# Kernel optimization log

Hardware: AMD Instinct MI355X
Metric: run time of the kernel (lower is better)

## Reference

```python
import jax, jax.numpy as jnp
import numpy as np

N_NODES = 100000
N_EDGES = 1600000
D_IN = 64
D_HID = 64
N_LAYERS = 3


def setup_inputs() -> dict:
    key = jax.random.key(0)
    ks = jax.random.split(key, 10)
    inp = {
        "node_feat": jax.random.normal(ks[0], (N_NODES, D_IN), dtype=jnp.float32),
        "src": jax.random.randint(ks[1], (N_EDGES,), 0, N_NODES, dtype=jnp.int32),
        "dst": jax.random.randint(ks[2], (N_EDGES,), 0, N_NODES, dtype=jnp.int32),
        "graph_len": jnp.ones((1,), dtype=jnp.int32) * N_NODES,
    }
    # GraphConv weights: shape (in_feats, out_feats), applied as feat @ W + b (DGL xavier-style init)
    dims = [D_IN] + [D_HID] * N_LAYERS
    for i in range(N_LAYERS):
        scale = float(np.sqrt(2.0 / (dims[i] + dims[i + 1])))
        inp[f"W{i}"] = jax.random.normal(ks[3 + i], (dims[i], dims[i + 1]), dtype=jnp.float32) * scale
        inp[f"b{i}"] = jnp.zeros((dims[i + 1],), dtype=jnp.float32)
    return inp


def reference(node_feat, src, dst, graph_len, W0, b0, W1, b1, W2, b2):
    n = node_feat.shape[0]
    e = src.shape[0]
    ones = jnp.ones((e,), dtype=node_feat.dtype)
    # DGL GraphConv norm='both': src-side out-degree^{-1/2}, dst-side in-degree^{-1/2}, clamp(min=1)
    deg_out = jax.ops.segment_sum(ones, src, num_segments=n)
    deg_in = jax.ops.segment_sum(ones, dst, num_segments=n)
    inv_sqrt_out = jax.lax.rsqrt(jnp.clip(deg_out, 1.0, None))[:, None]  # [N,1]
    inv_sqrt_in = jax.lax.rsqrt(jnp.clip(deg_in, 1.0, None))[:, None]    # [N,1]

    def graph_conv(x, W, b):
        msg = (x * inv_sqrt_out)[src]                              # [E,F] gather
        agg = jax.ops.segment_sum(msg, dst, num_segments=n)        # [N,F] scatter-add
        return (agg * inv_sqrt_in) @ W + b                         # SpMM result -> dense linear

    xs = []
    h = node_feat
    for W, b in ((W0, b0), (W1, b1), (W2, b2)):
        h = jax.nn.relu(graph_conv(h, W, b))
        xs.append(h)

    # Faithful to source: torch.sum(x, dim=1) -> per-node scalar [N]; concat over layers -> [3N]
    x_pool = jnp.concatenate([x.sum(axis=1) for x in xs], axis=-1)
    xs_cat = jnp.concatenate(xs, axis=-1)  # [N, 3*H]
    return x_pool, xs_cat
```

## Files before the change

kernel.cpp:

```cpp
#include <hip/hip_runtime.h>


#define TPB 256
#define CAPB 16384
#define CAP_S2 10240

__device__ __forceinline__ unsigned short f2bf(float f) {
  unsigned u = __float_as_uint(f);
  u += 0x7fff + ((u >> 16) & 1);
  return (unsigned short)(u >> 16);
}
__device__ __forceinline__ float bflo(unsigned u) { return __uint_as_float(u << 16); }
__device__ __forceinline__ float bfhi(unsigned u) { return __uint_as_float(u & 0xffff0000u); }

__global__ void init_cursors(int* __restrict__ cur_s, int* __restrict__ cur_d) {
  int t = threadIdx.x;
  cur_s[t] = t * CAPB;
  cur_d[t] = t * CAPB;
}

__global__ __launch_bounds__(256) void scatter_both(
    const int* __restrict__ src, const int* __restrict__ dst, int e,
    int* __restrict__ cur_s, int* __restrict__ cur_d,
    int* __restrict__ srcbuf, unsigned* __restrict__ edges1) {
  __shared__ int hs[256], hd[256];
  int t = threadIdx.x, b = blockIdx.x;
  hs[t] = 0; hd[t] = 0;
  __syncthreads();
  int base = b * 4096;
  int sv[16], dv[16];
  #pragma unroll
  for (int k = 0; k < 4; k++) {
    int i = base + 4 * t + 1024 * k;
    if (i + 3 < e) {
      int4 s4 = *(const int4*)&src[i];
      int4 d4 = *(const int4*)&dst[i];
      sv[4*k] = s4.x; sv[4*k+1] = s4.y; sv[4*k+2] = s4.z; sv[4*k+3] = s4.w;
      dv[4*k] = d4.x; dv[4*k+1] = d4.y; dv[4*k+2] = d4.z; dv[4*k+3] = d4.w;
    } else {
      #pragma unroll
      for (int j = 0; j < 4; j++) {
        int idx = i + j;
        if (idx < e) { sv[4*k+j] = src[idx]; dv[4*k+j] = dst[idx]; }
        else { sv[4*k+j] = -1; dv[4*k+j] = -1; }
      }
    }
  }
  #pragma unroll
  for (int k = 0; k < 16; k++) {
    if (dv[k] >= 0) {
      atomicAdd(&hs[sv[k] >> 9], 1);
      atomicAdd(&hd[dv[k] >> 9], 1);
    }
  }
  __syncthreads();
  int bs = hs[t], bd = hd[t];
  hs[t] = bs ? atomicAdd(&cur_s[t], bs) : 0;
  hd[t] = bd ? atomicAdd(&cur_d[t], bd) : 0;
  __syncthreads();
  #pragma unroll
  for (int k = 0; k < 16; k++) {
    if (dv[k] >= 0) {
      int ps = atomicAdd(&hs[sv[k] >> 9], 1);
      srcbuf[ps] = sv[k];
      int pd = atomicAdd(&hd[dv[k] >> 9], 1);
      edges1[pd] = ((unsigned)sv[k] << 9) | (unsigned)(dv[k] & 511);
    }
  }
}

__global__ __launch_bounds__(256) void sort_deg_cast(
    const unsigned* __restrict__ edges1, const int* __restrict__ srcbuf,
    const int* __restrict__ cur_s, const int* __restrict__ cur_d,
    const float* __restrict__ node_feat,
    int2* __restrict__ row_be,
    float* __restrict__ inv_in, float* __restrict__ inv_out,
    unsigned short* __restrict__ xb, int* __restrict__ col, int n) {
  __shared__ int sOut[CAP_S2];
  __shared__ int hist[512], cur[512];
  __shared__ int psum[256];
  __shared__ int dhist[512];
  __shared__ float sInv[512];
  int b = blockIdx.x, t = threadIdx.x;
  int sbase = b * CAPB;
  int es = cur_s[b];
  int ed = cur_d[b];
  int rstart = b << 9;
  int nrows = min(512, n - rstart);
  hist[t] = 0; hist[t + 256] = 0;
  dhist[t] = 0; dhist[t + 256] = 0;
  __syncthreads();
  for (int i = sbase + t; i < ed; i += TPB) atomicAdd(&hist[edges1[i] & 511u], 1);
  for (int i = sbase + t; i < es; i += TPB) atomicAdd(&dhist[srcbuf[i] & 511], 1);
  __syncthreads();
  #pragma unroll
  for (int k = 0; k < 2; k++) {
    int r = t + k * 256;
    if (r < nrows) {
      float iv = rsqrtf(fmaxf((float)dhist[r], 1.0f));
      sInv[r] = iv;
      inv_out[rstart + r] = iv;
    }
  }
  int h0 = hist[2 * t], h1 = hist[2 * t + 1];
  psum[t] = h0 + h1; __syncthreads();
  for (int off = 1; off < 256; off <<= 1) {
    int a = (t >= off) ? psum[t - off] : 0;
    __syncthreads(); psum[t] += a; __syncthreads();
  }
  int ex = psum[t] - (h0 + h1);
  cur[2 * t] = ex; cur[2 * t + 1] = ex + h0;
  if (2 * t < nrows) {
    row_be[rstart + 2 * t] = make_int2(sbase + ex, sbase + ex + h0);
    inv_in[rstart + 2 * t] = rsqrtf(fmaxf((float)h0, 1.0f));
  }
  if (2 * t + 1 < nrows) {
    row_be[rstart + 2 * t + 1] = make_int2(sbase + ex + h0, sbase + ex + h0 + h1);
    inv_in[rstart + 2 * t + 1] = rsqrtf(fmaxf((float)h1, 1.0f));
  }
  __syncthreads();
  for (int i = sbase + t; i < ed; i += TPB) {
    unsigned v = edges1[i];
    int pos = atomicAdd(&cur[v & 511u], 1);
    int svv = (int)(v >> 9);
    if (pos < CAP_S2) sOut[pos] = svv;
    else col[sbase + pos] = svv;
  }
  __syncthreads();
  int m = min(ed - sbase, CAP_S2);
  for (int k = t; k < m; k += TPB) col[sbase + k] = sOut[k];
  int total4 = nrows * 16;
  const float* xbase = node_feat + (size_t)rstart * 64;
  unsigned short* obase = xb + (size_t)rstart * 64;
  for (int u = t; u < total4; u += TPB) {
    int r = u >> 4;
    float sc = sInv[r];
    float4 v = *(const float4*)&xbase[(size_t)u * 4];
    ushort4 o;
    o.x = f2bf(v.x * sc); o.y = f2bf(v.y * sc);
    o.z = f2bf(v.z * sc); o.w = f2bf(v.w * sc);
    *(ushort4*)&obase[(size_t)u * 4] = o;
  }
}

__global__ __launch_bounds__(512) void spmm_gemm(
    const unsigned short* __restrict__ xb,
    const int2* __restrict__ row_be,
    const int* __restrict__ col,
    const float* __restrict__ inv_in, const float* __restrict__ inv_out,
    const float* __restrict__ W, const float* __restrict__ bias,
    float* __restrict__ out_cat, float* __restrict__ out_pool,
    unsigned short* __restrict__ xb_next, int n) {
  __shared__ float sXT[64][68];
  int t = threadIdx.x;
  int row0 = blockIdx.x << 6;
  int lane = t & 63;
  int g = lane >> 3;
  int l8 = (lane & 7) << 3;
  int wv = t >> 6;
  for (int k = 0; k < 8; k++) {
    int rl = wv * 8 + k;
    int row = row0 + rl;
    float v = 0.f;
    if (row < n) {
      int2 be = row_be[row];
      int s = be.x, e = be.y;
      float inv = inv_in[row];
      float a0 = 0, a1 = 0, a2 = 0, a3 = 0, a4 = 0, a5 = 0, a6 = 0, a7 = 0;
      int ec = e - 1;
      for (int i = s + g; i < e; i += 16) {
        int i1 = i + 8;
        int c0 = col[i];
        int c1 = col[min(i1, ec)];
        float m1 = (i1 < e) ? 1.f : 0.f;
        uint4 r0 = *(const uint4*)&xb[(size_t)c0 * 64 + l8];
        uint4 r1 = *(const uint4*)&xb[(size_t)c1 * 64 + l8];
        a0 += bflo(r0.x); a1 += bfhi(r0.x); a2 += bflo(r0.y); a3 += bfhi(r0.y);
        a4 += bflo(r0.z); a5 += bfhi(r0.z); a6 += bflo(r0.w); a7 += bfhi(r0.w);
        a0 = fmaf(m1, bflo(r1.x), a0); a1 = fmaf(m1, bfhi(r1.x), a1);
        a2 = fmaf(m1, bflo(r1.y), a2); a3 = fmaf(m1, bfhi(r1.y), a3);
        a4 = fmaf(m1, bflo(r1.z), a4); a5 = fmaf(m1, bfhi(r1.z), a5);
        a6 = fmaf(m1, bflo(r1.w), a6); a7 = fmaf(m1, bfhi(r1.w), a7);
      }
      a0 += __shfl_xor(a0, 8); a0 += __shfl_xor(a0, 16); a0 += __shfl_xor(a0, 32);
      a1 += __shfl_xor(a1, 8); a1 += __shfl_xor(a1, 16); a1 += __shfl_xor(a1, 32);
      a2 += __shfl_xor(a2, 8); a2 += __shfl_xor(a2, 16); a2 += __shfl_xor(a2, 32);
      a3 += __shfl_xor(a3, 8); a3 += __shfl_xor(a3, 16); a3 += __shfl_xor(a3, 32);
      a4 += __shfl_xor(a4, 8); a4 += __shfl_xor(a4, 16); a4 += __shfl_xor(a4, 32);
      a5 += __shfl_xor(a5, 8); a5 += __shfl_xor(a5, 16); a5 += __shfl_xor(a5, 32);
      a6 += __shfl_xor(a6, 8); a6 += __shfl_xor(a6, 16); a6 += __shfl_xor(a6, 32);
      a7 += __shfl_xor(a7, 8); a7 += __shfl_xor(a7, 16); a7 += __shfl_xor(a7, 32);
      float s0 = (g & 1) ? a1 : a0;
      float s1 = (g & 1) ? a3 : a2;
      float s2 = (g & 1) ? a5 : a4;
      float s3 = (g & 1) ? a7 : a6;
      float u0 = (g & 2) ? s1 : s0;
      float u1 = (g & 2) ? s3 : s2;
      v = ((g & 4) ? u1 : u0) * inv;
    }
    sXT[l8 + g][rl] = v;
  }
  __syncthreads();
  int tj = t & 15, tr = t >> 4;
  int j4 = tj << 2, r2 = tr << 1;
  const float4 bv = *(const float4*)&bias[j4];
  float4 a0 = bv, a1 = bv;
  #pragma unroll 8
  for (int f = 0; f < 64; f++) {
    float4 w  = *(const float4*)&W[f * 64 + j4];
    float2 xv = *(const float2*)&sXT[f][r2];
    a0.x = fmaf(xv.x, w.x, a0.x); a0.y = fmaf(xv.x, w.y, a0.y);
    a0.z = fmaf(xv.x, w.z, a0.z); a0.w = fmaf(xv.x, w.w, a0.w);
    a1.x = fmaf(xv.y, w.x, a1.x); a1.y = fmaf(xv.y, w.y, a1.y);
    a1.z = fmaf(xv.y, w.z, a1.z); a1.w = fmaf(xv.y, w.w, a1.w);
  }
  float4 accs[2] = {a0, a1};
  #pragma unroll
  for (int ri = 0; ri < 2; ri++) {
    int row = row0 + r2 + ri;
    if (row < n) {
      float4 h = accs[ri];
      h.x = fmaxf(h.x, 0.f); h.y = fmaxf(h.y, 0.f);
      h.z = fmaxf(h.z, 0.f); h.w = fmaxf(h.w, 0.f);
      *(float4*)&out_cat[(size_t)row * 192 + j4] = h;
      if (xb_next) {
        float sc = inv_out[row];
        ushort4 o;
        o.x = f2bf(h.x * sc); o.y = f2bf(h.y * sc);
        o.z = f2bf(h.z * sc); o.w = f2bf(h.w * sc);
        *(ushort4*)&xb_next[(size_t)row * 64 + j4] = o;
      }
      float part = h.x + h.y + h.z + h.w;
      part += __shfl_xor(part, 1);
      part += __shfl_xor(part, 2);
      part += __shfl_xor(part, 4);
      part += __shfl_xor(part, 8);
      if (tj == 0) out_pool[row] = part;
    }
  }
}


extern "C" void kernel_launch(void* const* d_in, const int* in_sizes, int n_in,
                              void* d_out, int out_size, void* d_ws, size_t ws_size,
                              hipStream_t stream) {
  const float* node_feat = (const float*)d_in[0];
  const int* src = (const int*)d_in[1];
  const int* dst = (const int*)d_in[2];
  const float* Ws[3] = {(const float*)d_in[4], (const float*)d_in[6], (const float*)d_in[8]};
  const float* bs[3] = {(const float*)d_in[5], (const float*)d_in[7], (const float*)d_in[9]};
  float* out = (float*)d_out;
  int n = in_sizes[0] / 64;
  int e = in_sizes[1];
  int nbb = (n + 511) >> 9;
  int nblk = (e + 4095) / 4096;
  size_t slots = (size_t)nbb * CAPB;

  char* p = (char*)d_ws;
  unsigned short* xba = (unsigned short*)p; p += (size_t)n * 64 * sizeof(unsigned short);
  unsigned short* xbb = (unsigned short*)p; p += (size_t)n * 64 * sizeof(unsigned short);
  float* inv_out = (float*)p;   p += (size_t)n * sizeof(float);
  float* inv_in = (float*)p;    p += (size_t)n * sizeof(float);
  int2* row_be = (int2*)p;      p += (size_t)n * sizeof(int2);
  int* cur_s = (int*)p;         p += 256 * sizeof(int);
  int* cur_d = (int*)p;         p += 256 * sizeof(int);
  unsigned* edges1 = (unsigned*)p; p += slots * sizeof(unsigned);
  int* srcbuf = (int*)p;        p += slots * sizeof(int);
  int* col = (int*)p;           p += slots * sizeof(int);

  init_cursors<<<1, 256, 0, stream>>>(cur_s, cur_d);
  scatter_both<<<nblk, TPB, 0, stream>>>(src, dst, e, cur_s, cur_d, srcbuf, edges1);
  sort_deg_cast<<<nbb, TPB, 0, stream>>>(edges1, srcbuf, cur_s, cur_d, node_feat,
                                         row_be, inv_in, inv_out, xba, col, n);

  float* cat_base = out + (size_t)3 * n;
  int nfb = (n + 63) >> 6;
  spmm_gemm<<<nfb, 512, 0, stream>>>(xba, row_be, col, inv_in, inv_out,
      Ws[0], bs[0], cat_base + 0 * 64, out + (size_t)0 * n, xbb, n);
  spmm_gemm<<<nfb, 512, 0, stream>>>(xbb, row_be, col, inv_in, inv_out,
      Ws[1], bs[1], cat_base + 1 * 64, out + (size_t)1 * n, xba, n);
  spmm_gemm<<<nfb, 512, 0, stream>>>(xba, row_be, col, inv_in, inv_out,
      Ws[2], bs[2], cat_base + 2 * 64, out + (size_t)2 * n, (unsigned short*)nullptr, n);
}
```

Measured before the change: 367.4 us.

## Compute out-degree with global atomics and shrink dst buckets to 256 rows

The out-degree bucketing pass (srcbuf scatter plus a per-bucket histogram) is replaced by direct global atomicAdd into a per-node deg_out array. Destination buckets shrink from 512 to 256 rows, so the sort kernel runs with twice as many blocks and half the shared-memory staging. The bf16 cast and scaling move into a separate grid-stride kernel. This removes one edge-sized scatter and read, but adds 1.6M global atomics and an extra kernel launch.

```diff
diff --git a/kernel.cpp b/kernel.cpp
--- a/kernel.cpp
+++ b/kernel.cpp
@@ -2,8 +2,8 @@
 
 
 #define TPB 256
-#define CAPB 16384
-#define CAP_S2 10240
+#define CAPB 8192
+#define CAP_S2 5120
 
 __device__ __forceinline__ unsigned short f2bf(float f) {
   unsigned u = __float_as_uint(f);
@@ -13,19 +13,23 @@
 __device__ __forceinline__ float bflo(unsigned u) { return __uint_as_float(u << 16); }
 __device__ __forceinline__ float bfhi(unsigned u) { return __uint_as_float(u & 0xffff0000u); }
 
-__global__ void init_cursors(int* __restrict__ cur_s, int* __restrict__ cur_d) {
+__global__ void init_zero(int* __restrict__ deg_out, int* __restrict__ cur_d, int n) {
   int t = threadIdx.x;
-  cur_s[t] = t * CAPB;
-  cur_d[t] = t * CAPB;
+  if (blockIdx.x == 0) {
+    cur_d[t] = t * CAPB;
+    cur_d[t + 256] = (t + 256) * CAPB;
+  }
+  int idx = blockIdx.x * 256 + t;
+  if (idx < n) deg_out[idx] = 0;
 }
 
 __global__ __launch_bounds__(256) void scatter_both(
     const int* __restrict__ src, const int* __restrict__ dst, int e,
-    int* __restrict__ cur_s, int* __restrict__ cur_d,
-    int* __restrict__ srcbuf, unsigned* __restrict__ edges1) {
-  __shared__ int hs[256], hd[256];
+    int* __restrict__ cur_d, int* __restrict__ deg_out,
+    unsigned* __restrict__ edges1) {
+  __shared__ int hd[512];
   int t = threadIdx.x, b = blockIdx.x;
-  hs[t] = 0; hd[t] = 0;
+  hd[t] = 0; hd[t + 256] = 0;
   __syncthreads();
   int base = b * 4096;
   int sv[16], dv[16];
@@ -49,97 +53,81 @@
   #pragma unroll
   for (int k = 0; k < 16; k++) {
     if (dv[k] >= 0) {
-      atomicAdd(&hs[sv[k] >> 9], 1);
-      atomicAdd(&hd[dv[k] >> 9], 1);
-    }
-  }
-  __syncthreads();
-  int bs = hs[t], bd = hd[t];
-  hs[t] = bs ? atomicAdd(&cur_s[t], bs) : 0;
-  hd[t] = bd ? atomicAdd(&cur_d[t], bd) : 0;
+      atomicAdd(&hd[dv[k] >> 8], 1);
+      atomicAdd(&deg_out[sv[k]], 1);
+    }
+  }
+  __syncthreads();
+  #pragma unroll
+  for (int k = 0; k < 2; k++) {
+    int bin = t + 256 * k;
+    int bd = hd[bin];
+    hd[bin] = bd ? atomicAdd(&cur_d[bin], bd) : 0;
+  }
   __syncthreads();
   #pragma unroll
   for (int k = 0; k < 16; k++) {
     if (dv[k] >= 0) {
-      int ps = atomicAdd(&hs[sv[k] >> 9], 1);
-      srcbuf[ps] = sv[k];
-      int pd = atomicAdd(&hd[dv[k] >> 9], 1);
-      edges1[pd] = ((unsigned)sv[k] << 9) | (unsigned)(dv[k] & 511);
-    }
-  }
-}
-
-__global__ __launch_bounds__(256) void sort_deg_cast(
-    const unsigned* __restrict__ edges1, const int* __restrict__ srcbuf,
-    const int* __restrict__ cur_s, const int* __restrict__ cur_d,
-    const float* __restrict__ node_feat,
-    int2* __restrict__ row_be,
-    float* __restrict__ inv_in, float* __restrict__ inv_out,
-    unsigned short* __restrict__ xb, int* __restrict__ col, int n) {
+      int pd = atomicAdd(&hd[dv[k] >> 8], 1);
+      edges1[pd] = ((unsigned)sv[k] << 8) | (unsigned)(dv[k] & 255);
+    }
+  }
+}
+
+__global__ __launch_bounds__(256) void sort_place(
+    const unsigned* __restrict__ edges1, const int* __restrict__ cur_d,
+    int2* __restrict__ row_be, float* __restrict__ inv_in,
+    int* __restrict__ col, int n) {
   __shared__ int sOut[CAP_S2];
-  __shared__ int hist[512], cur[512];
-  __shared__ int psum[256];
-  __shared__ int dhist[512];
-  __shared__ float sInv[512];
+  __shared__ int hist[256], cur[256], psum[256];
   int b = blockIdx.x, t = threadIdx.x;
   int sbase = b * CAPB;
-  int es = cur_s[b];
   int ed = cur_d[b];
-  int rstart = b << 9;
-  int nrows = min(512, n - rstart);
-  hist[t] = 0; hist[t + 256] = 0;
-  dhist[t] = 0; dhist[t + 256] = 0;
-  __syncthreads();
-  for (int i = sbase + t; i < ed; i += TPB) atomicAdd(&hist[edges1[i] & 511u], 1);
-  for (int i = sbase + t; i < es; i += TPB) atomicAdd(&dhist[srcbuf[i] & 511], 1);
-  __syncthreads();
-  #pragma unroll
-  for (int k = 0; k < 2; k++) {
-    int r = t + k * 256;
-    if (r < nrows) {
-      float iv = rsqrtf(fmaxf((float)dhist[r], 1.0f));
-      sInv[r] = iv;
-      inv_out[rstart + r] = iv;
-    }
-  }
-  int h0 = hist[2 * t], h1 = hist[2 * t + 1];
-  psum[t] = h0 + h1; __syncthreads();
+  int rstart = b << 8;
+  int nrows = min(256, n - rstart);
+  hist[t] = 0;
+  __syncthreads();
+  for (int i = sbase + t; i < ed; i += TPB) atomicAdd(&hist[edges1[i] & 255u], 1);
+  __syncthreads();
+  int h0 = hist[t];
+  psum[t] = h0; __syncthreads();
   for (int off = 1; off < 256; off <<= 1) {
     int a = (t >= off) ? psum[t - off] : 0;
     __syncthreads(); psum[t] += a; __syncthreads();
   }
-  int ex = psum[t] - (h0 + h1);
-  cur[2 * t] = ex; cur[2 * t + 1] = ex + h0;
-  if (2 * t < nrows) {
-    row_be[rstart + 2 * t] = make_int2(sbase + ex, sbase + ex + h0);
-    inv_in[rstart + 2 * t] = rsqrtf(fmaxf((float)h0, 1.0f));
-  }
-  if (2 * t + 1 < nrows) {
-    row_be[rstart + 2 * t + 1] = make_int2(sbase + ex + h0, sbase + ex + h0 + h1);
-    inv_in[rstart + 2 * t + 1] = rsqrtf(fmaxf((float)h1, 1.0f));
-  }
+  int ex = psum[t] - h0;
+  if (t < nrows) {
+    row_be[rstart + t] = make_int2(sbase + ex, sbase + ex + h0);
+    inv_in[rstart + t] = rsqrtf(fmaxf((float)h0, 1.0f));
+  }
+  cur[t] = ex;
   __syncthreads();
   for (int i = sbase + t; i < ed; i += TPB) {
     unsigned v = edges1[i];
-    int pos = atomicAdd(&cur[v & 511u], 1);
-    int svv = (int)(v >> 9);
+    int pos = atomicAdd(&cur[v & 255u], 1);
+    int svv = (int)(v >> 8);
     if (pos < CAP_S2) sOut[pos] = svv;
     else col[sbase + pos] = svv;
   }
   __syncthreads();
   int m = min(ed - sbase, CAP_S2);
   for (int k = t; k < m; k += TPB) col[sbase + k] = sOut[k];
-  int total4 = nrows * 16;
-  const float* xbase = node_feat + (size_t)rstart * 64;
-  unsigned short* obase = xb + (size_t)rstart * 64;
-  for (int u = t; u < total4; u += TPB) {
+}
+
+__global__ __launch_bounds__(256) void cast_xb(
+    const float* __restrict__ node_feat, const int* __restrict__ deg_out,
+    float* __restrict__ inv_out, unsigned short* __restrict__ xb, int n) {
+  int total4 = n * 16;
+  int stride = gridDim.x * 256;
+  for (int u = blockIdx.x * 256 + threadIdx.x; u < total4; u += stride) {
     int r = u >> 4;
-    float sc = sInv[r];
-    float4 v = *(const float4*)&xbase[(size_t)u * 4];
+    float iv = rsqrtf(fmaxf((float)deg_out[r], 1.0f));
+    if ((u & 15) == 0) inv_out[r] = iv;
+    float4 v = *(const float4*)&node_feat[(size_t)u * 4];
     ushort4 o;
-    o.x = f2bf(v.x * sc); o.y = f2bf(v.y * sc);
-    o.z = f2bf(v.z * sc); o.w = f2bf(v.w * sc);
-    *(ushort4*)&obase[(size_t)u * 4] = o;
+    o.x = f2bf(v.x * iv); o.y = f2bf(v.y * iv);
+    o.z = f2bf(v.z * iv); o.w = f2bf(v.w * iv);
+    *(ushort4*)&xb[(size_t)u * 4] = o;
   }
 }
 
@@ -252,7 +240,7 @@
   float* out = (float*)d_out;
   int n = in_sizes[0] / 64;
   int e = in_sizes[1];
-  int nbb = (n + 511) >> 9;
+  int nbb = (n + 255) >> 8;
   int nblk = (e + 4095) / 4096;
   size_t slots = (size_t)nbb * CAPB;
 
@@ -262,16 +250,15 @@
   float* inv_out = (float*)p;   p += (size_t)n * sizeof(float);
   float* inv_in = (float*)p;    p += (size_t)n * sizeof(float);
   int2* row_be = (int2*)p;      p += (size_t)n * sizeof(int2);
-  int* cur_s = (int*)p;         p += 256 * sizeof(int);
-  int* cur_d = (int*)p;         p += 256 * sizeof(int);
+  int* deg_out = (int*)p;       p += (size_t)n * sizeof(int);
+  int* cur_d = (int*)p;         p += 512 * sizeof(int);
   unsigned* edges1 = (unsigned*)p; p += slots * sizeof(unsigned);
-  int* srcbuf = (int*)p;        p += slots * sizeof(int);
   int* col = (int*)p;           p += slots * sizeof(int);
 
-  init_cursors<<<1, 256, 0, stream>>>(cur_s, cur_d);
-  scatter_both<<<nblk, TPB, 0, stream>>>(src, dst, e, cur_s, cur_d, srcbuf, edges1);
-  sort_deg_cast<<<nbb, TPB, 0, stream>>>(edges1, srcbuf, cur_s, cur_d, node_feat,
-                                         row_be, inv_in, inv_out, xba, col, n);
+  init_zero<<<(n + 255) / 256, 256, 0, stream>>>(deg_out, cur_d, n);
+  scatter_both<<<nblk, TPB, 0, stream>>>(src, dst, e, cur_d, deg_out, edges1);
+  sort_place<<<nbb, TPB, 0, stream>>>(edges1, cur_d, row_be, inv_in, col, n);
+  cast_xb<<<1024, 256, 0, stream>>>(node_feat, deg_out, inv_out, xba, n);
 
   float* cat_base = out + (size_t)3 * n;
   int nfb = (n + 63) >> 6;
```

Measured after the change: 399.1 us. +8.6%, slower.
